# Performance work log

Hardware: AMD Instinct MI355X
Metric: run time of the kernel (lower is better)

Reference implementation:

```python
import jax, jax.numpy as jnp
import numpy as np

E = 8        # n_routed_experts
Z = 4        # zero_expert_num (identity experts)
K = 2        # moe_topk
SCALE = 2.5  # routed_scaling_factor
T, H, I = 8192, 1024, 512


def setup_inputs() -> dict:
    key = jax.random.key(0)
    k0, k1, k2, k3, k4 = jax.random.split(key, 5)
    return {
        "hidden_states": jax.random.normal(k0, (T, H), jnp.float32),
        "router_w": jax.random.normal(k1, (E + Z, H), jnp.float32) * 0.02,
        "correction_bias": jax.random.normal(k2, (E + Z,), jnp.float32) * 0.01,
        "w13": jax.random.normal(k3, (E, 2 * I, H), jnp.float32) * 0.02,
        "w2": jax.random.normal(k4, (E, H, I), jnp.float32) * 0.02,
    }


def reference(hidden_states, router_w, correction_bias, w13, w2):
    # ---- router (float32) ----
    logits = hidden_states.astype(jnp.float32) @ router_w.T          # [T, E+Z]
    scores = jax.nn.softmax(logits, axis=-1)
    # correction bias only affects expert *selection*, not the gate weights
    _, topk_idx = jax.lax.top_k(scores + correction_bias, K)          # [T, K]
    topk_w = jnp.take_along_axis(scores, topk_idx, axis=-1)          # renormalize=False

    # ---- zero experts (identity type): idx >= E contributes scale * x ----
    is_zero = topk_idx >= E                                           # [T, K]
    routed_w = jnp.where(is_zero, 0.0, topk_w)
    zero_scale = jnp.where(is_zero, topk_w, 0.0).sum(-1, keepdims=True)
    zero_result = zero_scale * hidden_states                          # [T, H]

    # ---- combine weights per routed expert: [T, E] ----
    tok = jnp.arange(hidden_states.shape[0])[:, None]
    safe_idx = jnp.clip(topk_idx, 0, E - 1)   # zero-expert slots carry weight 0
    combine = jnp.zeros((hidden_states.shape[0], E), scores.dtype)
    combine = combine.at[tok, safe_idx].add(routed_w)

    # ---- grouped expert GEMMs (SiLU gated MLP), combined densely ----
    h = jnp.einsum('th,eih->eti', hidden_states, w13)                 # [E, T, 2I]
    g, u = jnp.split(h, 2, axis=-1)
    act = jax.nn.silu(g) * u                                          # [E, T, I]
    eo = jnp.einsum('eti,ehi->eth', act, w2)                          # [E, T, H]
    routed = jnp.einsum('te,eth->th', combine, eo)                    # [T, H]

    return routed * SCALE + zero_result
```

## Files before the change

kernel.cpp:

```cpp
#include <hip/hip_runtime.h>
#include <hip/hip_bf16.h>
#include <math.h>

typedef __bf16 bf16_t;
typedef bf16_t bf16x8 __attribute__((ext_vector_type(8)));
typedef float f32x4 __attribute__((ext_vector_type(4)));

#define T_TOK 8192
#define HDIM  1024
#define IDIM  512
#define NEXP  8
#define NTOT  12
#define MAXROWS (2 * T_TOK + NEXP * 128)
#define MAX_MTILES (MAXROWS / 128)

__device__ __forceinline__ void gll16(const bf16_t* g, bf16_t* l) {
  __builtin_amdgcn_global_load_lds((__attribute__((address_space(1))) void*)g,
                                   (__attribute__((address_space(3))) void*)l,
                                   16, 0, 0);
}

__global__ void cast_bf16_kernel(const float* __restrict__ in, bf16_t* __restrict__ out,
                                 size_t n8) {
  size_t gid = (size_t)blockIdx.x * blockDim.x + threadIdx.x;
  if (gid >= n8) return;
  size_t i = gid * 8;
  float4 a = *(const float4*)&in[i];
  float4 b = *(const float4*)&in[i + 4];
  bf16x8 o;
  o[0] = (bf16_t)a.x; o[1] = (bf16_t)a.y; o[2] = (bf16_t)a.z; o[3] = (bf16_t)a.w;
  o[4] = (bf16_t)b.x; o[5] = (bf16_t)b.y; o[6] = (bf16_t)b.z; o[7] = (bf16_t)b.w;
  *(bf16x8*)&out[i] = o;
}

__global__ void router_kernel(const float* __restrict__ x, const float* __restrict__ rw,
                              const float* __restrict__ bias,
                              int* __restrict__ tk_e, float* __restrict__ tk_w,
                              float* __restrict__ zscale) {
  int t = blockIdx.x;
  int l = threadIdx.x;
  const float4* xr = (const float4*)(x + (size_t)t * HDIM);
  float4 xv[4];
#pragma unroll
  for (int i = 0; i < 4; i++) xv[i] = xr[l + 64 * i];
  float part[NTOT];
#pragma unroll
  for (int e = 0; e < NTOT; e++) {
    const float4* wr = (const float4*)(rw + (size_t)e * HDIM);
    float s = 0.f;
#pragma unroll
    for (int i = 0; i < 4; i++) {
      float4 w = wr[l + 64 * i];
      s += xv[i].x * w.x + xv[i].y * w.y + xv[i].z * w.z + xv[i].w * w.w;
    }
    part[e] = s;
  }
#pragma unroll
  for (int off = 32; off > 0; off >>= 1)
#pragma unroll
    for (int e = 0; e < NTOT; e++) part[e] += __shfl_down(part[e], off);

  if (l == 0) {
    float mx = part[0];
#pragma unroll
    for (int e = 1; e < NTOT; e++) mx = fmaxf(mx, part[e]);
    float p[NTOT], den = 0.f;
#pragma unroll
    for (int e = 0; e < NTOT; e++) { p[e] = expf(part[e] - mx); den += p[e]; }
    float inv = 1.f / den;
#pragma unroll
    for (int e = 0; e < NTOT; e++) p[e] *= inv;
    float s0 = -1e30f, s1 = -1e30f; int i0 = 0, i1 = 0;
#pragma unroll
    for (int e = 0; e < NTOT; e++) {
      float v = p[e] + bias[e];
      if (v > s0) { s1 = s0; i1 = i0; s0 = v; i0 = e; }
      else if (v > s1) { s1 = v; i1 = e; }
    }
    float zs = 0.f;
    int idx[2] = { i0, i1 };
#pragma unroll
    for (int k = 0; k < 2; k++) {
      int e = idx[k];
      float w = p[e];
      if (e >= NEXP) { zs += w; tk_e[2 * t + k] = -1; tk_w[2 * t + k] = 0.f; }
      else           { tk_e[2 * t + k] = e; tk_w[2 * t + k] = w; }
    }
    zscale[t] = zs;
  }
}

__global__ void zero_init_kernel(int* __restrict__ counts, int* __restrict__ sel_tok,
                                 float* __restrict__ sel_w) {
  int i = blockIdx.x * blockDim.x + threadIdx.x;
  if (i < MAXROWS) { sel_tok[i] = 0; sel_w[i] = 0.f; }
  if (i < NEXP) counts[i] = 0;
}

__global__ void count_kernel(const int* __restrict__ tk_e, int* __restrict__ counts) {
  __shared__ int lc[NEXP];
  int tid = threadIdx.x;
  if (tid < NEXP) lc[tid] = 0;
  __syncthreads();
  int t = blockIdx.x * blockDim.x + tid;
  int e0 = tk_e[2 * t], e1 = tk_e[2 * t + 1];
  if (e0 >= 0) atomicAdd(&lc[e0], 1);
  if (e1 >= 0) atomicAdd(&lc[e1], 1);
  __syncthreads();
  if (tid < NEXP) atomicAdd(&counts[tid], lc[tid]);
}

__global__ void scan_kernel(const int* __restrict__ counts, int* __restrict__ off_pad,
                            int* __restrict__ cursor, int* __restrict__ total_rows,
                            int* __restrict__ tile_e, int* __restrict__ tile_p0,
                            int* __restrict__ n_mtiles) {
  if (threadIdx.x == 0) {
    int run = 0, nt = 0;
    for (int e = 0; e < NEXP; e++) {
      off_pad[e] = run;
      cursor[e] = run;
      int ntile = (counts[e] + 127) / 128;
      for (int i = 0; i < ntile; i++) {
        tile_e[nt] = e;
        tile_p0[nt] = run + i * 128;
        nt++;
      }
      run += ntile * 128;
    }
    *total_rows = run;
    *n_mtiles = nt;
  }
}

__global__ void assign_kernel(const int* __restrict__ tk_e, const float* __restrict__ tk_w,
                              int* __restrict__ cursor, int* __restrict__ sel_tok,
                              float* __restrict__ sel_w, int* __restrict__ pos) {
  __shared__ int lc[NEXP];
  __shared__ int lbase[NEXP];
  int tid = threadIdx.x;
  if (tid < NEXP) lc[tid] = 0;
  __syncthreads();
  int t = blockIdx.x * blockDim.x + tid;
  int e0 = tk_e[2 * t], e1 = tk_e[2 * t + 1];
  int r0 = (e0 >= 0) ? atomicAdd(&lc[e0], 1) : -1;
  int r1 = (e1 >= 0) ? atomicAdd(&lc[e1], 1) : -1;
  __syncthreads();
  if (tid < NEXP) lbase[tid] = atomicAdd(&cursor[tid], lc[tid]);
  __syncthreads();
  int p0 = -1, p1 = -1;
  if (e0 >= 0) { p0 = lbase[e0] + r0; sel_tok[p0] = t; sel_w[p0] = 2.5f * tk_w[2 * t]; }
  if (e1 >= 0) { p1 = lbase[e1] + r1; sel_tok[p1] = t; sel_w[p1] = 2.5f * tk_w[2 * t + 1]; }
  pos[2 * t] = p0;
  pos[2 * t + 1] = p1;
}

__global__ void gather_cast_kernel(const float* __restrict__ x, const int* __restrict__ sel_tok,
                                   const int* __restrict__ total_rows, bf16_t* __restrict__ xg) {
  size_t gid = (size_t)blockIdx.x * blockDim.x + threadIdx.x;
  size_t p = gid >> 7;
  if (p >= (size_t)*total_rows) return;
  size_t j = (gid & 127) << 3;
  int t = sel_tok[p];
  float4 a = *(const float4*)&x[(size_t)t * HDIM + j];
  float4 b = *(const float4*)&x[(size_t)t * HDIM + j + 4];
  bf16x8 o;
  o[0] = (bf16_t)a.x; o[1] = (bf16_t)a.y; o[2] = (bf16_t)a.z; o[3] = (bf16_t)a.w;
  o[4] = (bf16_t)b.x; o[5] = (bf16_t)b.y; o[6] = (bf16_t)b.z; o[7] = (bf16_t)b.w;
  *(bf16x8*)&xg[p * HDIM + j] = o;
}

__global__ __launch_bounds__(256) void gemm1_kernel(
    const bf16_t* __restrict__ xg, const bf16_t* __restrict__ w13b,
    const int* __restrict__ tile_e, const int* __restrict__ tile_p0,
    const int* __restrict__ n_mtiles, bf16_t* __restrict__ actb) {
  const int ti = blockIdx.x;
  if (ti >= *n_mtiles) return;
  const int e = tile_e[ti];
  const int p0 = tile_p0[ti];
  const int g0 = blockIdx.y * 64;

  __shared__ alignas(16) bf16_t As[128 * 32];
  __shared__ alignas(16) bf16_t Bs[128 * 32];
  const int tid = threadIdx.x;
  const int w = tid >> 6, l = tid & 63;
  const int wr = w >> 1, wc = w & 1;
  const int quad = l >> 4, c16 = l & 15;

  const int sr = w * 32 + (l >> 2);
  const int sc = (l & 3) * 8;
  const bf16_t* Ag0 = xg + (size_t)(p0 + sr) * HDIM + sc;
  const bf16_t* w13e = w13b + (size_t)e * (2 * IDIM) * HDIM;
  int r0 = sr, r1 = sr + 16;
  int col0 = g0 + (r0 >> 6) * 32 + (((r0 >> 4) & 1) * 16) + (r0 & 15) + (((r0 >> 5) & 1) ? IDIM : 0);
  int col1 = g0 + (r1 >> 6) * 32 + (((r1 >> 4) & 1) * 16) + (r1 & 15) + (((r1 >> 5) & 1) ? IDIM : 0);
  const bf16_t* Bg0 = w13e + (size_t)col0 * HDIM + sc;
  const bf16_t* Bg1 = w13e + (size_t)col1 * HDIM + sc;
  bf16_t* Al0 = &As[(w * 32) * 32];
  bf16_t* Bl0 = &Bs[(w * 32) * 32];

  f32x4 acc[4][4];
#pragma unroll
  for (int i = 0; i < 4; i++)
#pragma unroll
    for (int j = 0; j < 4; j++) acc[i][j] = (f32x4){0.f, 0.f, 0.f, 0.f};

  for (int k0 = 0; k0 < HDIM; k0 += 32) {
    gll16(Ag0 + k0, Al0);
    gll16(Ag0 + k0 + (size_t)16 * HDIM, Al0 + 16 * 32);
    gll16(Bg0 + k0, Bl0);
    gll16(Bg1 + k0, Bl0 + 16 * 32);
    __syncthreads();
    bf16x8 af[4], bfv[4];
#pragma unroll
    for (int mt = 0; mt < 4; mt++)
      af[mt] = *(const bf16x8*)&As[(wr * 64 + mt * 16 + c16) * 32 + quad * 8];
#pragma unroll
    for (int nt = 0; nt < 4; nt++)
      bfv[nt] = *(const bf16x8*)&Bs[(wc * 64 + nt * 16 + c16) * 32 + quad * 8];
#pragma unroll
    for (int mt = 0; mt < 4; mt++)
#pragma unroll
      for (int nt = 0; nt < 4; nt++)
        acc[mt][nt] = __builtin_amdgcn_mfma_f32_16x16x32_bf16(af[mt], bfv[nt], acc[mt][nt], 0, 0, 0);
    __syncthreads();
  }

#pragma unroll
  for (int mt = 0; mt < 4; mt++) {
    int rowb = p0 + wr * 64 + mt * 16 + quad * 4;
#pragma unroll
    for (int nt = 0; nt < 2; nt++) {
      int col = g0 + wc * 32 + nt * 16 + c16;
#pragma unroll
      for (int r = 0; r < 4; r++) {
        float g = acc[mt][nt][r];
        float u = acc[mt][nt + 2][r];
        float s = g / (1.f + expf(-g));
        actb[(size_t)(rowb + r) * IDIM + col] = (bf16_t)(s * u);
      }
    }
  }
}

__global__ __launch_bounds__(256) void gemm2_kernel(
    const bf16_t* __restrict__ actb, const bf16_t* __restrict__ w2b,
    const float* __restrict__ sel_w, const int* __restrict__ tile_e,
    const int* __restrict__ tile_p0, const int* __restrict__ n_mtiles,
    bf16_t* __restrict__ eob) {
  const int ti = blockIdx.x;
  if (ti >= *n_mtiles) return;
  const int e = tile_e[ti];
  const int p0 = tile_p0[ti];
  const int n0 = blockIdx.y * 128;

  __shared__ alignas(16) bf16_t As[128 * 32];
  __shared__ alignas(16) bf16_t Bs[128 * 32];
  const int tid = threadIdx.x;
  const int w = tid >> 6, l = tid & 63;
  const int wr = w >> 1, wc = w & 1;
  const int quad = l >> 4, c16 = l & 15;

  const int sr = w * 32 + (l >> 2);
  const int sc = (l & 3) * 8;
  const bf16_t* Ag0 = actb + (size_t)(p0 + sr) * IDIM + sc;
  const bf16_t* Bg0 = w2b + (size_t)e * HDIM * IDIM + (size_t)(n0 + sr) * IDIM + sc;
  bf16_t* Al0 = &As[(w * 32) * 32];
  bf16_t* Bl0 = &Bs[(w * 32) * 32];

  f32x4 acc[4][4];
#pragma unroll
  for (int i = 0; i < 4; i++)
#pragma unroll
    for (int j = 0; j < 4; j++) acc[i][j] = (f32x4){0.f, 0.f, 0.f, 0.f};

  for (int k0 = 0; k0 < IDIM; k0 += 32) {
    gll16(Ag0 + k0, Al0);
    gll16(Ag0 + k0 + (size_t)16 * IDIM, Al0 + 16 * 32);
    gll16(Bg0 + k0, Bl0);
    gll16(Bg0 + k0 + (size_t)16 * IDIM, Bl0 + 16 * 32);
    __syncthreads();
    bf16x8 af[4], bfv[4];
#pragma unroll
    for (int mt = 0; mt < 4; mt++)
      af[mt] = *(const bf16x8*)&As[(wr * 64 + mt * 16 + c16) * 32 + quad * 8];
#pragma unroll
    for (int nt = 0; nt < 4; nt++)
      bfv[nt] = *(const bf16x8*)&Bs[(wc * 64 + nt * 16 + c16) * 32 + quad * 8];
#pragma unroll
    for (int mt = 0; mt < 4; mt++)
#pragma unroll
      for (int nt = 0; nt < 4; nt++)
        acc[mt][nt] = __builtin_amdgcn_mfma_f32_16x16x32_bf16(af[mt], bfv[nt], acc[mt][nt], 0, 0, 0);
    __syncthreads();
  }

#pragma unroll
  for (int mt = 0; mt < 4; mt++) {
    int rowb = wr * 64 + mt * 16 + quad * 4;
    float cw[4];
#pragma unroll
    for (int r = 0; r < 4; r++) cw[r] = sel_w[p0 + rowb + r];
#pragma unroll
    for (int nt = 0; nt < 4; nt++) {
      int col = n0 + wc * 64 + nt * 16 + c16;
#pragma unroll
      for (int r = 0; r < 4; r++)
        eob[(size_t)(p0 + rowb + r) * HDIM + col] = (bf16_t)(cw[r] * acc[mt][nt][r]);
    }
  }
}

__global__ void combine_kernel(const float* __restrict__ x, const float* __restrict__ zscale,
                               const int* __restrict__ pos, const bf16_t* __restrict__ eob,
                               float* __restrict__ out) {
  size_t gid = (size_t)blockIdx.x * blockDim.x + threadIdx.x;
  size_t t = gid >> 7;
  size_t j = (gid & 127) << 3;
  float zs = zscale[t];
  int p0 = pos[2 * t], p1 = pos[2 * t + 1];
  float4 a = *(const float4*)&x[t * HDIM + j];
  float4 b = *(const float4*)&x[t * HDIM + j + 4];
  float o[8] = { zs * a.x, zs * a.y, zs * a.z, zs * a.w,
                 zs * b.x, zs * b.y, zs * b.z, zs * b.w };
  if (p0 >= 0) {
    bf16x8 v = *(const bf16x8*)&eob[(size_t)p0 * HDIM + j];
#pragma unroll
    for (int k = 0; k < 8; k++) o[k] += (float)v[k];
  }
  if (p1 >= 0) {
    bf16x8 v = *(const bf16x8*)&eob[(size_t)p1 * HDIM + j];
#pragma unroll
    for (int k = 0; k < 8; k++) o[k] += (float)v[k];
  }
  *(float4*)&out[t * HDIM + j] = make_float4(o[0], o[1], o[2], o[3]);
  *(float4*)&out[t * HDIM + j + 4] = make_float4(o[4], o[5], o[6], o[7]);
}

extern "C" void kernel_launch(void* const* d_in, const int* in_sizes, int n_in,
                              void* d_out, int out_size, void* d_ws, size_t ws_size,
                              hipStream_t stream) {
  const float* x    = (const float*)d_in[0];
  const float* rw   = (const float*)d_in[1];
  const float* bias = (const float*)d_in[2];
  const float* w13  = (const float*)d_in[3];
  const float* w2   = (const float*)d_in[4];
  float* out = (float*)d_out;

  char* ws = (char*)d_ws;
  bf16_t* w13b = (bf16_t*)ws;  ws += (size_t)NEXP * 2 * IDIM * HDIM * 2;
  bf16_t* w2b  = (bf16_t*)ws;  ws += (size_t)NEXP * HDIM * IDIM * 2;
  bf16_t* xg   = (bf16_t*)ws;  ws += (size_t)MAXROWS * HDIM * 2;
  bf16_t* actb = (bf16_t*)ws;  ws += (size_t)MAXROWS * IDIM * 2;
  bf16_t* eob  = (bf16_t*)ws;  ws += (size_t)MAXROWS * HDIM * 2;
  int*   tk_e    = (int*)ws;   ws += (size_t)T_TOK * 2 * 4;
  float* tk_w    = (float*)ws; ws += (size_t)T_TOK * 2 * 4;
  float* zscale  = (float*)ws; ws += (size_t)T_TOK * 4;
  int*   pos     = (int*)ws;   ws += (size_t)T_TOK * 2 * 4;
  int*   sel_tok = (int*)ws;   ws += (size_t)MAXROWS * 4;
  float* sel_w   = (float*)ws; ws += (size_t)MAXROWS * 4;
  int*   counts  = (int*)ws;   ws += NEXP * 4;
  int*   off_pad = (int*)ws;   ws += NEXP * 4;
  int*   cursor  = (int*)ws;   ws += NEXP * 4;
  int*   total_rows = (int*)ws; ws += 4;
  int*   tile_e  = (int*)ws;   ws += MAX_MTILES * 4;
  int*   tile_p0 = (int*)ws;   ws += MAX_MTILES * 4;
  int*   n_mtiles = (int*)ws;  ws += 4;

  {
    size_t n8 = (size_t)NEXP * 2 * IDIM * HDIM / 8;
    cast_bf16_kernel<<<(n8 + 255) / 256, 256, 0, stream>>>(w13, w13b, n8);
    n8 = (size_t)NEXP * HDIM * IDIM / 8;
    cast_bf16_kernel<<<(n8 + 255) / 256, 256, 0, stream>>>(w2, w2b, n8);
  }
  router_kernel<<<T_TOK, 64, 0, stream>>>(x, rw, bias, tk_e, tk_w, zscale);
  zero_init_kernel<<<(MAXROWS + 255) / 256, 256, 0, stream>>>(counts, sel_tok, sel_w);
  count_kernel<<<T_TOK / 256, 256, 0, stream>>>(tk_e, counts);
  scan_kernel<<<1, 64, 0, stream>>>(counts, off_pad, cursor, total_rows,
                                    tile_e, tile_p0, n_mtiles);
  assign_kernel<<<T_TOK / 256, 256, 0, stream>>>(tk_e, tk_w, cursor, sel_tok, sel_w, pos);
  gather_cast_kernel<<<(size_t)MAXROWS * (HDIM / 8) / 256, 256, 0, stream>>>(
      x, sel_tok, total_rows, xg);

  gemm1_kernel<<<dim3(MAX_MTILES, IDIM / 64), 256, 0, stream>>>(
      xg, w13b, tile_e, tile_p0, n_mtiles, actb);
  gemm2_kernel<<<dim3(MAX_MTILES, HDIM / 128), 256, 0, stream>>>(
      actb, w2b, sel_w, tile_e, tile_p0, n_mtiles, eob);

  combine_kernel<<<(size_t)T_TOK * HDIM / 8 / 256, 256, 0, stream>>>(
      x, zscale, pos, eob, out);
}
```

Baseline: 235.9 us.

## Fuse weight bf16 cast into GEMM tile loads with register-prefetched double-buffered LDS

Drops the separate fp32-to-bf16 weight cast kernels. The GEMMs now read fp32 weights directly and convert them while staging into a swizzled, double-buffered LDS tile, with the next K-slice prefetched through registers. Tile shapes shrink (BN 64, gemm1 at 32 gate columns per block), so there are more blocks and each block fetches weights redundantly across M tiles. The rest is smaller work: the full sel_tok/sel_w zero init is replaced by zeroing only the padding rows inside scan, and the router packs 4 tokens per block. The trade-off is that fp32 weights are re-read per M tile, roughly doubling weight traffic, in exchange for removing a full-weight cast pass.

After: 280.3 us. 1.19x slower.

```diff
diff --git a/kernel.cpp b/kernel.cpp
--- a/kernel.cpp
+++ b/kernel.cpp
@@ -13,32 +13,16 @@
 #define NTOT  12
 #define MAXROWS (2 * T_TOK + NEXP * 128)
 #define MAX_MTILES (MAXROWS / 128)
-
-__device__ __forceinline__ void gll16(const bf16_t* g, bf16_t* l) {
-  __builtin_amdgcn_global_load_lds((__attribute__((address_space(1))) void*)g,
-                                   (__attribute__((address_space(3))) void*)l,
-                                   16, 0, 0);
-}
-
-__global__ void cast_bf16_kernel(const float* __restrict__ in, bf16_t* __restrict__ out,
-                                 size_t n8) {
-  size_t gid = (size_t)blockIdx.x * blockDim.x + threadIdx.x;
-  if (gid >= n8) return;
-  size_t i = gid * 8;
-  float4 a = *(const float4*)&in[i];
-  float4 b = *(const float4*)&in[i + 4];
-  bf16x8 o;
-  o[0] = (bf16_t)a.x; o[1] = (bf16_t)a.y; o[2] = (bf16_t)a.z; o[3] = (bf16_t)a.w;
-  o[4] = (bf16_t)b.x; o[5] = (bf16_t)b.y; o[6] = (bf16_t)b.z; o[7] = (bf16_t)b.w;
-  *(bf16x8*)&out[i] = o;
-}
+#define BM 128
+#define BN 64
+#define BK 32
 
 __global__ void router_kernel(const float* __restrict__ x, const float* __restrict__ rw,
                               const float* __restrict__ bias,
                               int* __restrict__ tk_e, float* __restrict__ tk_w,
                               float* __restrict__ zscale) {
-  int t = blockIdx.x;
-  int l = threadIdx.x;
+  int t = blockIdx.x * 4 + (threadIdx.x >> 6);
+  int l = threadIdx.x & 63;
   const float4* xr = (const float4*)(x + (size_t)t * HDIM);
   float4 xv[4];
 #pragma unroll
@@ -90,11 +74,8 @@
   }
 }
 
-__global__ void zero_init_kernel(int* __restrict__ counts, int* __restrict__ sel_tok,
-                                 float* __restrict__ sel_w) {
-  int i = blockIdx.x * blockDim.x + threadIdx.x;
-  if (i < MAXROWS) { sel_tok[i] = 0; sel_w[i] = 0.f; }
-  if (i < NEXP) counts[i] = 0;
+__global__ void zero_counts_kernel(int* __restrict__ counts) {
+  if (threadIdx.x < NEXP) counts[threadIdx.x] = 0;
 }
 
 __global__ void count_kernel(const int* __restrict__ tk_e, int* __restrict__ counts) {
@@ -113,13 +94,16 @@
 __global__ void scan_kernel(const int* __restrict__ counts, int* __restrict__ off_pad,
                             int* __restrict__ cursor, int* __restrict__ total_rows,
                             int* __restrict__ tile_e, int* __restrict__ tile_p0,
-                            int* __restrict__ n_mtiles) {
+                            int* __restrict__ n_mtiles,
+                            int* __restrict__ sel_tok, float* __restrict__ sel_w) {
+  __shared__ int s_off[NEXP], s_cnt[NEXP];
   if (threadIdx.x == 0) {
     int run = 0, nt = 0;
     for (int e = 0; e < NEXP; e++) {
+      s_off[e] = run; s_cnt[e] = counts[e];
       off_pad[e] = run;
       cursor[e] = run;
-      int ntile = (counts[e] + 127) / 128;
+      int ntile = (s_cnt[e] + 127) / 128;
       for (int i = 0; i < ntile; i++) {
         tile_e[nt] = e;
         tile_p0[nt] = run + i * 128;
@@ -129,6 +113,14 @@
     }
     *total_rows = run;
     *n_mtiles = nt;
+  }
+  __syncthreads();
+  for (int i = threadIdx.x; i < NEXP * 128; i += blockDim.x) {
+    int e = i >> 7, idx = i & 127;
+    int c = s_cnt[e];
+    int padded = ((c + 127) / 128) * 128;
+    int pos = c + idx;
+    if (pos < padded) { sel_tok[s_off[e] + pos] = 0; sel_w[s_off[e] + pos] = 0.f; }
   }
 }
 
@@ -169,81 +161,131 @@
   *(bf16x8*)&xg[p * HDIM + j] = o;
 }
 
+__device__ __forceinline__ bf16x8 cvt8(float4 f0, float4 f1) {
+  bf16x8 t;
+  t[0] = (bf16_t)f0.x; t[1] = (bf16_t)f0.y; t[2] = (bf16_t)f0.z; t[3] = (bf16_t)f0.w;
+  t[4] = (bf16_t)f1.x; t[5] = (bf16_t)f1.y; t[6] = (bf16_t)f1.z; t[7] = (bf16_t)f1.w;
+  return t;
+}
+
 __global__ __launch_bounds__(256) void gemm1_kernel(
-    const bf16_t* __restrict__ xg, const bf16_t* __restrict__ w13b,
+    const bf16_t* __restrict__ xg, const float* __restrict__ w13,
     const int* __restrict__ tile_e, const int* __restrict__ tile_p0,
     const int* __restrict__ n_mtiles, bf16_t* __restrict__ actb) {
   const int ti = blockIdx.x;
   if (ti >= *n_mtiles) return;
   const int e = tile_e[ti];
   const int p0 = tile_p0[ti];
-  const int g0 = blockIdx.y * 64;
-
-  __shared__ alignas(16) bf16_t As[128 * 32];
-  __shared__ alignas(16) bf16_t Bs[128 * 32];
+  const int g0 = blockIdx.y * 32;
+
+  __shared__ alignas(16) bf16_t As[2][BM * BK];
+  __shared__ alignas(16) bf16_t Bs[2][BN * BK];
+
   const int tid = threadIdx.x;
   const int w = tid >> 6, l = tid & 63;
-  const int wr = w >> 1, wc = w & 1;
   const int quad = l >> 4, c16 = l & 15;
 
-  const int sr = w * 32 + (l >> 2);
-  const int sc = (l & 3) * 8;
-  const bf16_t* Ag0 = xg + (size_t)(p0 + sr) * HDIM + sc;
-  const bf16_t* w13e = w13b + (size_t)e * (2 * IDIM) * HDIM;
-  int r0 = sr, r1 = sr + 16;
-  int col0 = g0 + (r0 >> 6) * 32 + (((r0 >> 4) & 1) * 16) + (r0 & 15) + (((r0 >> 5) & 1) ? IDIM : 0);
-  int col1 = g0 + (r1 >> 6) * 32 + (((r1 >> 4) & 1) * 16) + (r1 & 15) + (((r1 >> 5) & 1) ? IDIM : 0);
-  const bf16_t* Bg0 = w13e + (size_t)col0 * HDIM + sc;
-  const bf16_t* Bg1 = w13e + (size_t)col1 * HDIM + sc;
-  bf16_t* Al0 = &As[(w * 32) * 32];
-  bf16_t* Bl0 = &Bs[(w * 32) * 32];
-
-  f32x4 acc[4][4];
-#pragma unroll
-  for (int i = 0; i < 4; i++)
+  const int ar = tid >> 1;
+  const int ac2 = (tid & 1) * 2;
+  const int swzA = (ar >> 1) & 3;
+  const bf16_t* Ap = xg + (size_t)(p0 + ar) * HDIM + ac2 * 8;
+  const int aw0 = ar * BK + ((ac2 ^ swzA) * 8);
+  const int aw1 = ar * BK + (((ac2 + 1) ^ swzA) * 8);
+
+  const int br = tid >> 2;
+  const int bc = tid & 3;
+  const int wcol = g0 + (br & 31) + ((br >> 5) ? IDIM : 0);
+  const float* Bp = w13 + (size_t)e * (2 * IDIM) * HDIM + (size_t)wcol * HDIM + bc * 8;
+  const int bw0 = br * BK + ((bc ^ ((br >> 1) & 3)) * 8);
+
+  f32x4 acc[2][4];
+#pragma unroll
+  for (int i = 0; i < 2; i++)
 #pragma unroll
     for (int j = 0; j < 4; j++) acc[i][j] = (f32x4){0.f, 0.f, 0.f, 0.f};
 
-  for (int k0 = 0; k0 < HDIM; k0 += 32) {
-    gll16(Ag0 + k0, Al0);
-    gll16(Ag0 + k0 + (size_t)16 * HDIM, Al0 + 16 * 32);
-    gll16(Bg0 + k0, Bl0);
-    gll16(Bg1 + k0, Bl0 + 16 * 32);
+  int aoff[2], boff[4];
+#pragma unroll
+  for (int mt = 0; mt < 2; mt++) {
+    int r = w * 32 + mt * 16 + c16;
+    aoff[mt] = r * BK + ((quad ^ ((r >> 1) & 3)) * 8);
+  }
+#pragma unroll
+  for (int nt = 0; nt < 4; nt++) {
+    int r = nt * 16 + c16;
+    boff[nt] = r * BK + ((quad ^ ((r >> 1) & 3)) * 8);
+  }
+
+  int4 a0, a1; float4 b0, b1;
+  a0 = *(const int4*)(Ap);
+  a1 = *(const int4*)(Ap + 8);
+  b0 = *(const float4*)(Bp);
+  b1 = *(const float4*)(Bp + 4);
+  *(int4*)&As[0][aw0] = a0;
+  *(int4*)&As[0][aw1] = a1;
+  *(bf16x8*)&Bs[0][bw0] = cvt8(b0, b1);
+  __syncthreads();
+
+  int p = 0;
+  for (int t = 1; t < HDIM / BK; ++t) {
+    const int k0 = t * BK;
+    a0 = *(const int4*)(Ap + k0);
+    a1 = *(const int4*)(Ap + k0 + 8);
+    b0 = *(const float4*)(Bp + k0);
+    b1 = *(const float4*)(Bp + k0 + 4);
+    {
+      const bf16_t* Asp = As[p];
+      const bf16_t* Bsp = Bs[p];
+      bf16x8 af[2], bfv[4];
+#pragma unroll
+      for (int mt = 0; mt < 2; mt++) af[mt] = *(const bf16x8*)&Asp[aoff[mt]];
+#pragma unroll
+      for (int nt = 0; nt < 4; nt++) bfv[nt] = *(const bf16x8*)&Bsp[boff[nt]];
+#pragma unroll
+      for (int mt = 0; mt < 2; mt++)
+#pragma unroll
+        for (int nt = 0; nt < 4; nt++)
+          acc[mt][nt] = __builtin_amdgcn_mfma_f32_16x16x32_bf16(af[mt], bfv[nt], acc[mt][nt], 0, 0, 0);
+    }
+    *(int4*)&As[p ^ 1][aw0] = a0;
+    *(int4*)&As[p ^ 1][aw1] = a1;
+    *(bf16x8*)&Bs[p ^ 1][bw0] = cvt8(b0, b1);
     __syncthreads();
-    bf16x8 af[4], bfv[4];
-#pragma unroll
-    for (int mt = 0; mt < 4; mt++)
-      af[mt] = *(const bf16x8*)&As[(wr * 64 + mt * 16 + c16) * 32 + quad * 8];
-#pragma unroll
-    for (int nt = 0; nt < 4; nt++)
-      bfv[nt] = *(const bf16x8*)&Bs[(wc * 64 + nt * 16 + c16) * 32 + quad * 8];
-#pragma unroll
-    for (int mt = 0; mt < 4; mt++)
+    p ^= 1;
+  }
+  {
+    const bf16_t* Asp = As[p];
+    const bf16_t* Bsp = Bs[p];
+    bf16x8 af[2], bfv[4];
+#pragma unroll
+    for (int mt = 0; mt < 2; mt++) af[mt] = *(const bf16x8*)&Asp[aoff[mt]];
+#pragma unroll
+    for (int nt = 0; nt < 4; nt++) bfv[nt] = *(const bf16x8*)&Bsp[boff[nt]];
+#pragma unroll
+    for (int mt = 0; mt < 2; mt++)
 #pragma unroll
       for (int nt = 0; nt < 4; nt++)
         acc[mt][nt] = __builtin_amdgcn_mfma_f32_16x16x32_bf16(af[mt], bfv[nt], acc[mt][nt], 0, 0, 0);
-    __syncthreads();
-  }
-
-#pragma unroll
-  for (int mt = 0; mt < 4; mt++) {
-    int rowb = p0 + wr * 64 + mt * 16 + quad * 4;
+  }
+
+#pragma unroll
+  for (int mt = 0; mt < 2; mt++) {
+    int rowb = p0 + w * 32 + mt * 16 + quad * 4;
 #pragma unroll
     for (int nt = 0; nt < 2; nt++) {
-      int col = g0 + wc * 32 + nt * 16 + c16;
+      int col = g0 + nt * 16 + c16;
 #pragma unroll
       for (int r = 0; r < 4; r++) {
         float g = acc[mt][nt][r];
         float u = acc[mt][nt + 2][r];
-        float s = g / (1.f + expf(-g));
-        actb[(size_t)(rowb + r) * IDIM + col] = (bf16_t)(s * u);
+        actb[(size_t)(rowb + r) * IDIM + col] = (bf16_t)(g / (1.f + expf(-g)) * u);
       }
     }
   }
 }
 
 __global__ __launch_bounds__(256) void gemm2_kernel(
-    const bf16_t* __restrict__ actb, const bf16_t* __restrict__ w2b,
+    const bf16_t* __restrict__ actb, const float* __restrict__ w2,
     const float* __restrict__ sel_w, const int* __restrict__ tile_e,
     const int* __restrict__ tile_p0, const int* __restrict__ n_mtiles,
     bf16_t* __restrict__ eob) {
@@ -251,58 +293,106 @@
   if (ti >= *n_mtiles) return;
   const int e = tile_e[ti];
   const int p0 = tile_p0[ti];
-  const int n0 = blockIdx.y * 128;
-
-  __shared__ alignas(16) bf16_t As[128 * 32];
-  __shared__ alignas(16) bf16_t Bs[128 * 32];
+  const int n0 = blockIdx.y * BN;
+
+  __shared__ alignas(16) bf16_t As[2][BM * BK];
+  __shared__ alignas(16) bf16_t Bs[2][BN * BK];
+
   const int tid = threadIdx.x;
   const int w = tid >> 6, l = tid & 63;
-  const int wr = w >> 1, wc = w & 1;
   const int quad = l >> 4, c16 = l & 15;
 
-  const int sr = w * 32 + (l >> 2);
-  const int sc = (l & 3) * 8;
-  const bf16_t* Ag0 = actb + (size_t)(p0 + sr) * IDIM + sc;
-  const bf16_t* Bg0 = w2b + (size_t)e * HDIM * IDIM + (size_t)(n0 + sr) * IDIM + sc;
-  bf16_t* Al0 = &As[(w * 32) * 32];
-  bf16_t* Bl0 = &Bs[(w * 32) * 32];
-
-  f32x4 acc[4][4];
-#pragma unroll
-  for (int i = 0; i < 4; i++)
+  const int ar = tid >> 1;
+  const int ac2 = (tid & 1) * 2;
+  const int swzA = (ar >> 1) & 3;
+  const bf16_t* Ap = actb + (size_t)(p0 + ar) * IDIM + ac2 * 8;
+  const int aw0 = ar * BK + ((ac2 ^ swzA) * 8);
+  const int aw1 = ar * BK + (((ac2 + 1) ^ swzA) * 8);
+
+  const int br = tid >> 2;
+  const int bc = tid & 3;
+  const float* Bp = w2 + (size_t)e * HDIM * IDIM + (size_t)(n0 + br) * IDIM + bc * 8;
+  const int bw0 = br * BK + ((bc ^ ((br >> 1) & 3)) * 8);
+
+  f32x4 acc[2][4];
+#pragma unroll
+  for (int i = 0; i < 2; i++)
 #pragma unroll
     for (int j = 0; j < 4; j++) acc[i][j] = (f32x4){0.f, 0.f, 0.f, 0.f};
 
-  for (int k0 = 0; k0 < IDIM; k0 += 32) {
-    gll16(Ag0 + k0, Al0);
-    gll16(Ag0 + k0 + (size_t)16 * IDIM, Al0 + 16 * 32);
-    gll16(Bg0 + k0, Bl0);
-    gll16(Bg0 + k0 + (size_t)16 * IDIM, Bl0 + 16 * 32);
+  int aoff[2], boff[4];
+#pragma unroll
+  for (int mt = 0; mt < 2; mt++) {
+    int r = w * 32 + mt * 16 + c16;
+    aoff[mt] = r * BK + ((quad ^ ((r >> 1) & 3)) * 8);
+  }
+#pragma unroll
+  for (int nt = 0; nt < 4; nt++) {
+    int r = nt * 16 + c16;
+    boff[nt] = r * BK + ((quad ^ ((r >> 1) & 3)) * 8);
+  }
+
+  int4 a0, a1; float4 b0, b1;
+  a0 = *(const int4*)(Ap);
+  a1 = *(const int4*)(Ap + 8);
+  b0 = *(const float4*)(Bp);
+  b1 = *(const float4*)(Bp + 4);
+  *(int4*)&As[0][aw0] = a0;
+  *(int4*)&As[0][aw1] = a1;
+  *(bf16x8*)&Bs[0][bw0] = cvt8(b0, b1);
+  __syncthreads();
+
+  int p = 0;
+  for (int t = 1; t < IDIM / BK; ++t) {
+    const int k0 = t * BK;
+    a0 = *(const int4*)(Ap + k0);
+    a1 = *(const int4*)(Ap + k0 + 8);
+    b0 = *(const float4*)(Bp + k0);
+    b1 = *(const float4*)(Bp + k0 + 4);
+    {
+      const bf16_t* Asp = As[p];
+      const bf16_t* Bsp = Bs[p];
+      bf16x8 af[2], bfv[4];
+#pragma unroll
+      for (int mt = 0; mt < 2; mt++) af[mt] = *(const bf16x8*)&Asp[aoff[mt]];
+#pragma unroll
+      for (int nt = 0; nt < 4; nt++) bfv[nt] = *(const bf16x8*)&Bsp[boff[nt]];
+#pragma unroll
+      for (int mt = 0; mt < 2; mt++)
+#pragma unroll
+        for (int nt = 0; nt < 4; nt++)
+          acc[mt][nt] = __builtin_amdgcn_mfma_f32_16x16x32_bf16(af[mt], bfv[nt], acc[mt][nt], 0, 0, 0);
+    }
+    *(int4*)&As[p ^ 1][aw0] = a0;
+    *(int4*)&As[p ^ 1][aw1] = a1;
+    *(bf16x8*)&Bs[p ^ 1][bw0] = cvt8(b0, b1);
     __syncthreads();
-    bf16x8 af[4], bfv[4];
-#pragma unroll
-    for (int mt = 0; mt < 4; mt++)
-      af[mt] = *(const bf16x8*)&As[(wr * 64 + mt * 16 + c16) * 32 + quad * 8];
-#pragma unroll
-    for (int nt = 0; nt < 4; nt++)
-      bfv[nt] = *(const bf16x8*)&Bs[(wc * 64 + nt * 16 + c16) * 32 + quad * 8];
-#pragma unroll
-    for (int mt = 0; mt < 4; mt++)
+    p ^= 1;
+  }
+  {
+    const bf16_t* Asp = As[p];
+    const bf16_t* Bsp = Bs[p];
+    bf16x8 af[2], bfv[4];
+#pragma unroll
+    for (int mt = 0; mt < 2; mt++) af[mt] = *(const bf16x8*)&Asp[aoff[mt]];
+#pragma unroll
+    for (int nt = 0; nt < 4; nt++) bfv[nt] = *(const bf16x8*)&Bsp[boff[nt]];
+#pragma unroll
+    for (int mt = 0; mt < 2; mt++)
 #pragma unroll
       for (int nt = 0; nt < 4; nt++)
         acc[mt][nt] = __builtin_amdgcn_mfma_f32_16x16x32_bf16(af[mt], bfv[nt], acc[mt][nt], 0, 0, 0);
-    __syncthreads();
-  }
-
-#pragma unroll
-  for (int mt = 0; mt < 4; mt++) {
-    int rowb = wr * 64 + mt * 16 + quad * 4;
+  }
+
+#pragma unroll
+  for (int mt = 0; mt < 2; mt++) {
+    int rowb = w * 32 + mt * 16 + quad * 4;
     float cw[4];
 #pragma unroll
     for (int r = 0; r < 4; r++) cw[r] = sel_w[p0 + rowb + r];
 #pragma unroll
     for (int nt = 0; nt < 4; nt++) {
-      int col = n0 + wc * 64 + nt * 16 + c16;
+      int col = n0 + nt * 16 + c16;
 #pragma unroll
       for (int r = 0; r < 4; r++)
         eob[(size_t)(p0 + rowb + r) * HDIM + col] = (bf16_t)(cw[r] * acc[mt][nt][r]);
@@ -347,8 +437,6 @@
   float* out = (float*)d_out;
 
   char* ws = (char*)d_ws;
-  bf16_t* w13b = (bf16_t*)ws;  ws += (size_t)NEXP * 2 * IDIM * HDIM * 2;
-  bf16_t* w2b  = (bf16_t*)ws;  ws += (size_t)NEXP * HDIM * IDIM * 2;
   bf16_t* xg   = (bf16_t*)ws;  ws += (size_t)MAXROWS * HDIM * 2;
   bf16_t* actb = (bf16_t*)ws;  ws += (size_t)MAXROWS * IDIM * 2;
   bf16_t* eob  = (bf16_t*)ws;  ws += (size_t)MAXROWS * HDIM * 2;
@@ -366,25 +454,19 @@
   int*   tile_p0 = (int*)ws;   ws += MAX_MTILES * 4;
   int*   n_mtiles = (int*)ws;  ws += 4;
 
-  {
-    size_t n8 = (size_t)NEXP * 2 * IDIM * HDIM / 8;
-    cast_bf16_kernel<<<(n8 + 255) / 256, 256, 0, stream>>>(w13, w13b, n8);
-    n8 = (size_t)NEXP * HDIM * IDIM / 8;
-    cast_bf16_kernel<<<(n8 + 255) / 256, 256, 0, stream>>>(w2, w2b, n8);
-  }
-  router_kernel<<<T_TOK, 64, 0, stream>>>(x, rw, bias, tk_e, tk_w, zscale);
-  zero_init_kernel<<<(MAXROWS + 255) / 256, 256, 0, stream>>>(counts, sel_tok, sel_w);
+  zero_counts_kernel<<<1, 64, 0, stream>>>(counts);
+  router_kernel<<<T_TOK / 4, 256, 0, stream>>>(x, rw, bias, tk_e, tk_w, zscale);
   count_kernel<<<T_TOK / 256, 256, 0, stream>>>(tk_e, counts);
-  scan_kernel<<<1, 64, 0, stream>>>(counts, off_pad, cursor, total_rows,
-                                    tile_e, tile_p0, n_mtiles);
+  scan_kernel<<<1, 256, 0, stream>>>(counts, off_pad, cursor, total_rows,
+                                     tile_e, tile_p0, n_mtiles, sel_tok, sel_w);
   assign_kernel<<<T_TOK / 256, 256, 0, stream>>>(tk_e, tk_w, cursor, sel_tok, sel_w, pos);
   gather_cast_kernel<<<(size_t)MAXROWS * (HDIM / 8) / 256, 256, 0, stream>>>(
       x, sel_tok, total_rows, xg);
 
-  gemm1_kernel<<<dim3(MAX_MTILES, IDIM / 64), 256, 0, stream>>>(
-      xg, w13b, tile_e, tile_p0, n_mtiles, actb);
-  gemm2_kernel<<<dim3(MAX_MTILES, HDIM / 128), 256, 0, stream>>>(
-      actb, w2b, sel_w, tile_e, tile_p0, n_mtiles, eob);
+  gemm1_kernel<<<dim3(MAX_MTILES, IDIM / 32), 256, 0, stream>>>(
+      xg, w13, tile_e, tile_p0, n_mtiles, actb);
+  gemm2_kernel<<<dim3(MAX_MTILES, HDIM / BN), 256, 0, stream>>>(
+      actb, w2, sel_w, tile_e, tile_p0, n_mtiles, eob);
 
   combine_kernel<<<(size_t)T_TOK * HDIM / 8 / 256, 256, 0, stream>>>(
       x, zscale, pos, eob, out);
```
